# Performance work log

Hardware: AMD Instinct MI355X
Metric: run time of the kernel (lower is better)

The kernel has to match this reference:

```python
import jax, jax.numpy as jnp
import numpy as np

NUM_NODES = 100000
NUM_EDGES = 1600000
DIM = 64
NUM_LAYERS = 3


def setup_inputs() -> dict:
    key = jax.random.key(0)
    k1, k2 = jax.random.split(key)
    x = jax.random.normal(k1, (NUM_NODES, DIM), dtype=jnp.float32)
    adj_t = jax.random.randint(k2, (2, NUM_EDGES), 0, NUM_NODES, dtype=jnp.int64)
    return {"x": x, "adj_t": adj_t}


def reference(x, adj_t):
    n = x.shape[0]
    # undirected -> add reversed edges (adj_t_is_undirected=True path)
    edge_index = jnp.concatenate([adj_t, adj_t[::-1]], axis=1)  # [2, 2E]
    row, col = edge_index[0], edge_index[1]
    edge_weight = jnp.ones((row.shape[0],), dtype=x.dtype)
    # gcn_norm: D^-0.5 A D^-0.5 (degree computed by scatter over col)
    deg = jax.ops.segment_sum(edge_weight, col, num_segments=n)
    deg_inv_sqrt = jnp.where(deg > 0, jax.lax.rsqrt(deg), 0.0).astype(x.dtype)
    w = deg_inv_sqrt[row] * edge_weight * deg_inv_sqrt[col]  # [2E]
    outs = [x]
    for _ in range(NUM_LAYERS):
        # gather -> scale -> scatter_add (SpMM)
        msgs = w[:, None] * x[row]                     # [2E, D]
        x = jax.ops.segment_sum(msgs, col, num_segments=n)  # [N, D]
        outs.append(x)
    return jnp.mean(jnp.stack(outs), axis=0)
```

## Files before the change

kernel.cpp:

```cpp
#include <hip/hip_runtime.h>

#define DIM 64
#define BKT_SHIFT 7
#define BKT_G 128
#define NBLK 256
#define HIST_B 1024
#define SCAP (HIST_B * 8)
#define CAP 4608
#define RCAP 18

__device__ inline float blo(unsigned p) { return __uint_as_float(p << 16); }
__device__ inline float bhi(unsigned p) { return __uint_as_float(p & 0xffff0000u); }
__device__ inline unsigned bpack(float x, float y) {
    unsigned ux = __float_as_uint(x);
    unsigned uy = __float_as_uint(y);
    ux += 0x7fffu + ((ux >> 16) & 1u);
    uy += 0x7fffu + ((uy >> 16) & 1u);
    return (ux >> 16) | (uy & 0xffff0000u);
}

__global__ void zero_kernel(int* __restrict__ p, int n) {
    int i = blockIdx.x * blockDim.x + threadIdx.x;
    if (i < n) p[i] = 0;
}

__global__ __launch_bounds__(HIST_B)
void place_direct_kernel(const int* __restrict__ adj, int E,
                         int* __restrict__ gcnt,
                         unsigned* __restrict__ pairs, int NB) {
    extern __shared__ int L[];
    int* cnt    = L;
    int* lb     = L + NB;
    int* cur    = L + 2 * NB + 1;
    int* gb     = L + 3 * NB + 1;
    int* wsum   = L + 4 * NB + 1;
    int* staged = L + 4 * NB + 17;
    const int tid  = threadIdx.x;
    const int lane = tid & 63;
    const int wid  = tid >> 6;
    const int n4 = E >> 2;
    const int4* srcs = (const int4*)adj;
    const int4* dsts = (const int4*)(adj + E);
    const int nrounds = (n4 + NBLK * HIST_B - 1) / (NBLK * HIST_B);

    for (int r = 0; r < nrounds; ++r) {
        for (int g = tid; g < NB; g += HIST_B) cnt[g] = 0;
        __syncthreads();
        int i = (r * NBLK + blockIdx.x) * HIST_B + tid;
        int4 a = {0, 0, 0, 0}, b = {0, 0, 0, 0};
        int valid = 0;
        if (i < n4) {
            a = srcs[i];
            b = dsts[i];
            valid = 1;
            atomicAdd(&cnt[a.x >> BKT_SHIFT], 1);
            atomicAdd(&cnt[a.y >> BKT_SHIFT], 1);
            atomicAdd(&cnt[a.z >> BKT_SHIFT], 1);
            atomicAdd(&cnt[a.w >> BKT_SHIFT], 1);
            atomicAdd(&cnt[b.x >> BKT_SHIFT], 1);
            atomicAdd(&cnt[b.y >> BKT_SHIFT], 1);
            atomicAdd(&cnt[b.z >> BKT_SHIFT], 1);
            atomicAdd(&cnt[b.w >> BKT_SHIFT], 1);
        }
        __syncthreads();
        int v = (tid < NB) ? cnt[tid] : 0;
        int s = v;
#pragma unroll
        for (int off = 1; off < 64; off <<= 1) {
            int o = __shfl_up(s, off);
            if (lane >= off) s += o;
        }
        if (lane == 63) wsum[wid] = s;
        __syncthreads();
        if (wid == 0 && lane < 16) {
            int w = wsum[lane];
#pragma unroll
            for (int off = 1; off < 16; off <<= 1) {
                int o = __shfl_up(w, off);
                if (lane >= off) w += o;
            }
            wsum[lane] = w;
        }
        __syncthreads();
        int incl = s + (wid ? wsum[wid - 1] : 0);
        if (tid < NB) {
            lb[tid + 1] = incl;
            cur[tid] = incl - v;
            gb[tid]  = (v > 0) ? atomicAdd(&gcnt[tid], v) : 0;
        }
        if (tid == 0) lb[0] = 0;
        __syncthreads();
        int total = lb[NB];
        if (valid) {
#define STAGE_EMIT(av, bv)                                                     \
    {                                                                          \
        int g_ = (bv) >> BKT_SHIFT;                                            \
        int p_ = atomicAdd(&cur[g_], 1);                                       \
        staged[p_] = (int)(((unsigned)((bv) & (BKT_G - 1)) << 17) |            \
                           (unsigned)(av));                                    \
        g_ = (av) >> BKT_SHIFT;                                                \
        p_ = atomicAdd(&cur[g_], 1);                                           \
        staged[p_] = (int)(((unsigned)((av) & (BKT_G - 1)) << 17) |            \
                           (unsigned)(bv));                                    \
    }
            STAGE_EMIT(a.x, b.x); STAGE_EMIT(a.y, b.y);
            STAGE_EMIT(a.z, b.z); STAGE_EMIT(a.w, b.w);
#undef STAGE_EMIT
        }
        __syncthreads();
        for (int k = tid; k < total; k += HIST_B) {
            int lo = 0, hi = NB - 1;
            while (lo < hi) {
                int mid = (lo + hi + 1) >> 1;
                if (lb[mid] <= k) lo = mid; else hi = mid - 1;
            }
            int p = gb[lo] + (k - lb[lo]);
            if (p < CAP)
                pairs[(size_t)lo * CAP + p] = (unsigned)staged[k];
        }
        __syncthreads();
    }
    if (blockIdx.x == 0) {
        for (int e = (n4 << 2) + tid; e < E; e += HIST_B) {
            int av = adj[e], bv = adj[E + e];
            int g1 = bv >> BKT_SHIFT;
            int p1 = atomicAdd(&gcnt[g1], 1);
            if (p1 < CAP)
                pairs[(size_t)g1 * CAP + p1] =
                    ((unsigned)(bv & (BKT_G - 1)) << 17) | (unsigned)av;
            int g2 = av >> BKT_SHIFT;
            int p2 = atomicAdd(&gcnt[g2], 1);
            if (p2 < CAP)
                pairs[(size_t)g2 * CAP + p2] =
                    ((unsigned)(av & (BKT_G - 1)) << 17) | (unsigned)bv;
        }
    }
}

__global__ __launch_bounds__(256)
void pass2_build_kernel(const unsigned* __restrict__ pairs,
                        const int* __restrict__ gcnt,
                        const float4* __restrict__ x,
                        int* __restrict__ csr_src,
                        int* __restrict__ row_ptr,
                        int* __restrict__ deg,
                        float* __restrict__ dinv,
                        uint4* __restrict__ xs0,
                        int N, int NB, int total_adj) {
    __shared__ int cnt[BKT_G];
    __shared__ int pre[BKT_G];
    __shared__ int cur[BKT_G];
    __shared__ float dv[BKT_G];
    __shared__ int win[CAP];
    __shared__ int red[256];
    int g = blockIdx.x;
    int base = g << BKT_SHIFT;
    size_t poff = (size_t)g * CAP;
    int m = gcnt[g];
    if (m > CAP) m = CAP;
    int lsum = 0;
    for (int h = threadIdx.x; h < g; h += 256) lsum += gcnt[h];
    red[threadIdx.x] = lsum;
    if (threadIdx.x < BKT_G) cnt[threadIdx.x] = 0;
    __syncthreads();
    for (int o = 128; o > 0; o >>= 1) {
        if (threadIdx.x < o) red[threadIdx.x] += red[threadIdx.x + o];
        __syncthreads();
    }
    int coff = red[0];
    unsigned rec[RCAP];
#pragma unroll
    for (int k = 0; k < RCAP; ++k) {
        int i = threadIdx.x + k * 256;
        unsigned p = 0;
        if (i < m) {
            p = pairs[poff + i];
            atomicAdd(&cnt[p >> 17], 1);
        }
        rec[k] = p;
    }
    __syncthreads();
    if (threadIdx.x < BKT_G) pre[threadIdx.x] = cnt[threadIdx.x];
    __syncthreads();
    for (int o = 1; o < BKT_G; o <<= 1) {
        int t = 0;
        if (threadIdx.x < BKT_G && threadIdx.x >= o) t = pre[threadIdx.x - o];
        __syncthreads();
        if (threadIdx.x < BKT_G) pre[threadIdx.x] += t;
        __syncthreads();
    }
    if (threadIdx.x < BKT_G) {
        int v = base + threadIdx.x;
        if (v < N) {
            int c = cnt[threadIdx.x];
            int lstart = pre[threadIdx.x] - c;
            float di = (c > 0) ? rsqrtf((float)c) : 0.0f;
            row_ptr[v] = coff + lstart;
            deg[v] = c;
            dinv[v] = di;
            dv[threadIdx.x] = di;
            cur[threadIdx.x] = lstart;
        }
    }
    if (g == NB - 1 && threadIdx.x == 0) row_ptr[N] = total_adj;
    __syncthreads();
#pragma unroll
    for (int k = 0; k < RCAP; ++k) {
        int i = threadIdx.x + k * 256;
        if (i < m) {
            unsigned p = rec[k];
            int pos = atomicAdd(&cur[p >> 17], 1);
            win[pos] = (int)(p & 0x1ffffu);
        }
    }
    __syncthreads();
    for (int i = threadIdx.x; i < m; i += 256)
        csr_src[coff + i] = win[i];
    for (int w = threadIdx.x; w < BKT_G * 8; w += blockDim.x) {
        int vl = w >> 3, sub = w & 7;
        int v = base + vl;
        if (v < N) {
            float di = dv[vl];
            float4 xa = x[(size_t)v * 16 + sub * 2];
            float4 xb = x[(size_t)v * 16 + sub * 2 + 1];
            uint4 o;
            o.x = bpack(di * xa.x, di * xa.y);
            o.y = bpack(di * xa.z, di * xa.w);
            o.z = bpack(di * xb.x, di * xb.y);
            o.w = bpack(di * xb.z, di * xb.w);
            xs0[(size_t)v * 8 + sub] = o;
        }
    }
}

#define SPMM_ACCUM_BODY                                                        \
    int half = threadIdx.x & 31;                                               \
    int nb = half >> 3, sub = half & 7;                                        \
    int beg = row_ptr[v];                                                      \
    int end = row_ptr[v + 1];                                                  \
    int full = (end - beg) >> 4;                                               \
    float a0 = 0, a1 = 0, a2 = 0, a3 = 0, a4 = 0, a5 = 0, a6 = 0, a7 = 0;      \
    int j = beg;                                                               \
    int s0 = 0, s1 = 0, s2 = 0, s3 = 0;                                        \
    if (full > 0) {                                                            \
        int b = j + 4 * nb;                                                    \
        s0 = csr_src[b];     s1 = csr_src[b + 1];                              \
        s2 = csr_src[b + 2]; s3 = csr_src[b + 3];                              \
    }                                                                          \
    for (int it = 0; it < full; ++it) {                                        \
        int jn = j + 16;                                                       \
        int t0 = 0, t1 = 0, t2 = 0, t3 = 0;                                    \
        if (it + 1 < full) {                                                   \
            int b = jn + 4 * nb;                                               \
            t0 = csr_src[b];     t1 = csr_src[b + 1];                          \
            t2 = csr_src[b + 2]; t3 = csr_src[b + 3];                          \
        }                                                                      \
        uint4 p0 = xs_in[(size_t)s0 * 8 + sub];                                \
        uint4 p1 = xs_in[(size_t)s1 * 8 + sub];                                \
        uint4 p2 = xs_in[(size_t)s2 * 8 + sub];                                \
        uint4 p3 = xs_in[(size_t)s3 * 8 + sub];                                \
        a0 += (blo(p0.x) + blo(p1.x)) + (blo(p2.x) + blo(p3.x));               \
        a1 += (bhi(p0.x) + bhi(p1.x)) + (bhi(p2.x) + bhi(p3.x));               \
        a2 += (blo(p0.y) + blo(p1.y)) + (blo(p2.y) + blo(p3.y));               \
        a3 += (bhi(p0.y) + bhi(p1.y)) + (bhi(p2.y) + bhi(p3.y));               \
        a4 += (blo(p0.z) + blo(p1.z)) + (blo(p2.z) + blo(p3.z));               \
        a5 += (bhi(p0.z) + bhi(p1.z)) + (bhi(p2.z) + bhi(p3.z));               \
        a6 += (blo(p0.w) + blo(p1.w)) + (blo(p2.w) + blo(p3.w));               \
        a7 += (bhi(p0.w) + bhi(p1.w)) + (bhi(p2.w) + bhi(p3.w));               \
        s0 = t0; s1 = t1; s2 = t2; s3 = t3;                                    \
        j = jn;                                                                \
    }                                                                          \
    for (int idx = j + nb; idx < end; idx += 4) {                              \
        int s = csr_src[idx];                                                  \
        uint4 p = xs_in[(size_t)s * 8 + sub];                                  \
        a0 += blo(p.x); a1 += bhi(p.x);                                        \
        a2 += blo(p.y); a3 += bhi(p.y);                                        \
        a4 += blo(p.z); a5 += bhi(p.z);                                        \
        a6 += blo(p.w); a7 += bhi(p.w);                                        \
    }                                                                          \
    a0 += __shfl_xor(a0, 8);  a0 += __shfl_xor(a0, 16);                        \
    a1 += __shfl_xor(a1, 8);  a1 += __shfl_xor(a1, 16);                        \
    a2 += __shfl_xor(a2, 8);  a2 += __shfl_xor(a2, 16);                        \
    a3 += __shfl_xor(a3, 8);  a3 += __shfl_xor(a3, 16);                        \
    a4 += __shfl_xor(a4, 8);  a4 += __shfl_xor(a4, 16);                        \
    a5 += __shfl_xor(a5, 8);  a5 += __shfl_xor(a5, 16);                        \
    a6 += __shfl_xor(a6, 8);  a6 += __shfl_xor(a6, 16);                        \
    a7 += __shfl_xor(a7, 8);  a7 += __shfl_xor(a7, 16);

__global__ void spmm_bf16_kernel(const int* __restrict__ row_ptr,
                                 const int* __restrict__ csr_src,
                                 const float* __restrict__ dinv,
                                 const uint4* __restrict__ xs_in,
                                 uint4* __restrict__ xs_out, int N) {
    int t = blockIdx.x * blockDim.x + threadIdx.x;
    int v = t >> 5;
    if (v >= N) return;
    SPMM_ACCUM_BODY
    if (nb == 0) {
        float di = dinv[v];
        float d2 = di * di;
        uint4 o;
        o.x = bpack(d2 * a0, d2 * a1);
        o.y = bpack(d2 * a2, d2 * a3);
        o.z = bpack(d2 * a4, d2 * a5);
        o.w = bpack(d2 * a6, d2 * a7);
        xs_out[(size_t)v * 8 + sub] = o;
    }
}

__global__ void spmm_last_kernel(const int* __restrict__ row_ptr,
                                 const int* __restrict__ csr_src,
                                 const float* __restrict__ dinv,
                                 const int* __restrict__ deg,
                                 const uint4* __restrict__ xs_in,
                                 const uint4* __restrict__ xs1,
                                 const float4* __restrict__ x,
                                 float4* __restrict__ out, int N) {
    int t = blockIdx.x * blockDim.x + threadIdx.x;
    int v = t >> 5;
    if (v >= N) return;
    SPMM_ACCUM_BODY
    if (nb == 0) {
        float di = dinv[v];
        float rs = sqrtf((float)deg[v]);
        size_t idx = (size_t)v * 8 + sub;
        uint4 q1 = xs1[idx];
        uint4 q2 = xs_in[idx];
        float4 xa = x[(size_t)v * 16 + sub * 2];
        float4 xb = x[(size_t)v * 16 + sub * 2 + 1];
        float4 oa, ob;
        oa.x = 0.25f * (xa.x + rs * (blo(q1.x) + blo(q2.x)) + di * a0);
        oa.y = 0.25f * (xa.y + rs * (bhi(q1.x) + bhi(q2.x)) + di * a1);
        oa.z = 0.25f * (xa.z + rs * (blo(q1.y) + blo(q2.y)) + di * a2);
        oa.w = 0.25f * (xa.w + rs * (bhi(q1.y) + bhi(q2.y)) + di * a3);
        ob.x = 0.25f * (xb.x + rs * (blo(q1.z) + blo(q2.z)) + di * a4);
        ob.y = 0.25f * (xb.y + rs * (bhi(q1.z) + bhi(q2.z)) + di * a5);
        ob.z = 0.25f * (xb.z + rs * (blo(q1.w) + blo(q2.w)) + di * a6);
        ob.w = 0.25f * (xb.w + rs * (bhi(q1.w) + bhi(q2.w)) + di * a7);
        out[(size_t)v * 16 + sub * 2]     = oa;
        out[(size_t)v * 16 + sub * 2 + 1] = ob;
    }
}

extern "C" void kernel_launch(void* const* d_in, const int* in_sizes, int n_in,
                              void* d_out, int out_size, void* d_ws, size_t ws_size,
                              hipStream_t stream) {
    const float* x = (const float*)d_in[0];
    const int* adj = (const int*)d_in[1];
    float* out     = (float*)d_out;

    const int total_adj = in_sizes[1];
    const int E = total_adj / 2;
    const int N = in_sizes[0] / DIM;
    const int NB = (N + BKT_G - 1) / BKT_G;

    size_t BUF = (size_t)total_adj * 4;
    size_t xsb = (size_t)N * 32 * 4;
    if (xsb > BUF) BUF = xsb;
    BUF = (BUF + 255) & ~(size_t)255;
    size_t PAIRS_B = ((size_t)NB * CAP * 4 + 255) & ~(size_t)255;

    char* ws = (char*)d_ws;
    int*      deg     = (int*)(ws);
    float*    dinv    = (float*)(ws + (size_t)512 * 1024);
    int*      row_ptr = (int*)(ws + (size_t)1024 * 1024);
    int*      gcnt    = (int*)(ws + (size_t)1536 * 1024);
    char*     big     = ws + (size_t)1664 * 1024;
    int*      csr_src = (int*)(big);
    unsigned* pairs   = (unsigned*)(big + BUF);
    uint4*    xs0     = (uint4*)(big + BUF + PAIRS_B);
    uint4*    xs1     = (uint4*)(big + BUF + PAIRS_B + BUF);
    uint4*    xs2     = (uint4*)(big + BUF + PAIRS_B + 2 * BUF);

    const int B = 256;

    zero_kernel<<<(NB + 1023) / 1024, 1024, 0, stream>>>(gcnt, NB);

    size_t place_lds = (size_t)(4 * NB + 17 + SCAP) * sizeof(int);
    place_direct_kernel<<<NBLK, HIST_B, place_lds, stream>>>(adj, E, gcnt,
                                                             pairs, NB);

    pass2_build_kernel<<<NB, B, 0, stream>>>(pairs, gcnt, (const float4*)x,
                                             csr_src, row_ptr, deg, dinv,
                                             xs0, N, NB, total_adj);

    const int nblocks32 = (int)(((long long)N * 32 + B - 1) / B);
    spmm_bf16_kernel<<<nblocks32, B, 0, stream>>>(row_ptr, csr_src, dinv, xs0, xs1, N);
    spmm_bf16_kernel<<<nblocks32, B, 0, stream>>>(row_ptr, csr_src, dinv, xs1, xs2, N);
    spmm_last_kernel<<<nblocks32, B, 0, stream>>>(row_ptr, csr_src, dinv, deg,
                                                  xs2, xs1, (const float4*)x,
                                                  (float4*)out, N);
}
```

Before: 280.2 us.

## Sort CSR neighbors by source octant and gather per-octant for cache locality

The CSR build now sorts each row's neighbors by a 3-bit source-range key, splitting sources into 8 octants. It stores per-node octant prefix counts packed as bytes in a new qpre array. The SpMM kernels are rewritten so each block handles 64 nodes and walks the octants in order, with a block barrier between octants, so gathers of source features stay within one smaller slice of the feature table and should hit L2 more often. The thread mapping also changes to one 32-bit word (two bf16 features) per lane per node, in place of 16-byte vector loads split over neighbor quarters. The price is narrower loads, serial per-node edge loops, extra barriers, and byte-packed counts that overflow if a node's degree exceeds 255.

```diff
diff --git a/kernel.cpp b/kernel.cpp
--- a/kernel.cpp
+++ b/kernel.cpp
@@ -8,6 +8,8 @@
 #define SCAP (HIST_B * 8)
 #define CAP 4608
 #define RCAP 18
+#define NKEY (BKT_G * 8)
+#define NPB 64
 
 __device__ inline float blo(unsigned p) { return __uint_as_float(p << 16); }
 __device__ inline float bhi(unsigned p) { return __uint_as_float(p & 0xffff0000u); }
@@ -145,14 +147,16 @@
                         int* __restrict__ row_ptr,
                         int* __restrict__ deg,
                         float* __restrict__ dinv,
+                        uint2* __restrict__ qpre,
                         uint4* __restrict__ xs0,
                         int N, int NB, int total_adj) {
-    __shared__ int cnt[BKT_G];
-    __shared__ int pre[BKT_G];
-    __shared__ int cur[BKT_G];
+    __shared__ int cnt[NKEY];
+    __shared__ int pre[NKEY];
+    __shared__ int cur[NKEY];
     __shared__ float dv[BKT_G];
     __shared__ int win[CAP];
     __shared__ int red[256];
+    __shared__ int wsum4[4];
     int g = blockIdx.x;
     int base = g << BKT_SHIFT;
     size_t poff = (size_t)g * CAP;
@@ -161,7 +165,7 @@
     int lsum = 0;
     for (int h = threadIdx.x; h < g; h += 256) lsum += gcnt[h];
     red[threadIdx.x] = lsum;
-    if (threadIdx.x < BKT_G) cnt[threadIdx.x] = 0;
+    for (int kk = threadIdx.x; kk < NKEY; kk += 256) cnt[kk] = 0;
     __syncthreads();
     for (int o = 128; o > 0; o >>= 1) {
         if (threadIdx.x < o) red[threadIdx.x] += red[threadIdx.x + o];
@@ -175,31 +179,66 @@
         unsigned p = 0;
         if (i < m) {
             p = pairs[poff + i];
-            atomicAdd(&cnt[p >> 17], 1);
+            int key = (int)(((p >> 17) << 3) | ((p & 0x1ffffu) >> 14));
+            atomicAdd(&cnt[key], 1);
         }
         rec[k] = p;
     }
     __syncthreads();
-    if (threadIdx.x < BKT_G) pre[threadIdx.x] = cnt[threadIdx.x];
-    __syncthreads();
-    for (int o = 1; o < BKT_G; o <<= 1) {
-        int t = 0;
-        if (threadIdx.x < BKT_G && threadIdx.x >= o) t = pre[threadIdx.x - o];
-        __syncthreads();
-        if (threadIdx.x < BKT_G) pre[threadIdx.x] += t;
-        __syncthreads();
-    }
+    {
+        int lane = threadIdx.x & 63, wid = threadIdx.x >> 6;
+        int t4 = threadIdx.x << 2;
+        int c0 = cnt[t4], c1 = cnt[t4 + 1], c2 = cnt[t4 + 2], c3 = cnt[t4 + 3];
+        int i1 = c0 + c1, i2 = i1 + c2, i3 = i2 + c3;
+        int s = i3;
+#pragma unroll
+        for (int off = 1; off < 64; off <<= 1) {
+            int o = __shfl_up(s, off);
+            if (lane >= off) s += o;
+        }
+        if (lane == 63) wsum4[wid] = s;
+        __syncthreads();
+        if (threadIdx.x == 0) {
+            int w0 = wsum4[0], w1 = wsum4[1], w2 = wsum4[2];
+            wsum4[0] = 0; wsum4[1] = w0; wsum4[2] = w0 + w1;
+            wsum4[3] = w0 + w1 + w2;
+        }
+        __syncthreads();
+        int texc = wsum4[wid] + s - i3;
+        pre[t4]     = texc + c0;
+        pre[t4 + 1] = texc + i1;
+        pre[t4 + 2] = texc + i2;
+        pre[t4 + 3] = texc + i3;
+        cur[t4]     = texc;
+        cur[t4 + 1] = texc + c0;
+        cur[t4 + 2] = texc + i1;
+        cur[t4 + 3] = texc + i2;
+    }
+    __syncthreads();
     if (threadIdx.x < BKT_G) {
         int v = base + threadIdx.x;
         if (v < N) {
-            int c = cnt[threadIdx.x];
-            int lstart = pre[threadIdx.x] - c;
+            int k8 = threadIdx.x << 3;
+            int nstart = threadIdx.x ? pre[k8 - 1] : 0;
+            int b0 = pre[k8]     - nstart;
+            int b1 = pre[k8 + 1] - nstart;
+            int b2 = pre[k8 + 2] - nstart;
+            int b3 = pre[k8 + 3] - nstart;
+            int b4 = pre[k8 + 4] - nstart;
+            int b5 = pre[k8 + 5] - nstart;
+            int b6 = pre[k8 + 6] - nstart;
+            int b7 = pre[k8 + 7] - nstart;
+            int c = b7;
             float di = (c > 0) ? rsqrtf((float)c) : 0.0f;
-            row_ptr[v] = coff + lstart;
+            row_ptr[v] = coff + nstart;
             deg[v] = c;
             dinv[v] = di;
             dv[threadIdx.x] = di;
-            cur[threadIdx.x] = lstart;
+            qpre[v] = make_uint2(
+                (unsigned)b0 | ((unsigned)b1 << 8) | ((unsigned)b2 << 16) |
+                    ((unsigned)b3 << 24),
+                (unsigned)b4 | ((unsigned)b5 << 8) | ((unsigned)b6 << 16) |
+                    ((unsigned)b7 << 24));
         }
     }
     if (g == NB - 1 && threadIdx.x == 0) row_ptr[N] = total_adj;
@@ -209,7 +248,8 @@
         int i = threadIdx.x + k * 256;
         if (i < m) {
             unsigned p = rec[k];
-            int pos = atomicAdd(&cur[p >> 17], 1);
+            int key = (int)(((p >> 17) << 3) | ((p & 0x1ffffu) >> 14));
+            int pos = atomicAdd(&cur[key], 1);
             win[pos] = (int)(p & 0x1ffffu);
         }
     }
@@ -233,112 +273,110 @@
     }
 }
 
-#define SPMM_ACCUM_BODY                                                        \
-    int half = threadIdx.x & 31;                                               \
-    int nb = half >> 3, sub = half & 7;                                        \
-    int beg = row_ptr[v];                                                      \
-    int end = row_ptr[v + 1];                                                  \
-    int full = (end - beg) >> 4;                                               \
-    float a0 = 0, a1 = 0, a2 = 0, a3 = 0, a4 = 0, a5 = 0, a6 = 0, a7 = 0;      \
-    int j = beg;                                                               \
-    int s0 = 0, s1 = 0, s2 = 0, s3 = 0;                                        \
-    if (full > 0) {                                                            \
-        int b = j + 4 * nb;                                                    \
-        s0 = csr_src[b];     s1 = csr_src[b + 1];                              \
-        s2 = csr_src[b + 2]; s3 = csr_src[b + 3];                              \
+#define SPMM_OCT_GATHER                                                        \
+    int lane = threadIdx.x & 31;                                               \
+    int grp  = threadIdx.x >> 5;                                               \
+    float ax[8] = {0, 0, 0, 0, 0, 0, 0, 0};                                    \
+    float ay[8] = {0, 0, 0, 0, 0, 0, 0, 0};                                    \
+    for (int oct = 0; oct < 8; ++oct) {                                        \
+        _Pragma("unroll")                                                      \
+        for (int k = 0; k < 8; ++k) {                                          \
+            int ni = k * 8 + grp;                                              \
+            int v = v0 + ni;                                                   \
+            if (v < N) {                                                       \
+                unsigned long long Q =                                         \
+                    ((unsigned long long)qb[ni] << 32) | qa[ni];               \
+                int hi = (int)((Q >> (oct * 8)) & 255ull);                     \
+                int lo = oct ? (int)((Q >> (oct * 8 - 8)) & 255ull) : 0;       \
+                int bs = rp[ni] + lo;                                          \
+                int len = hi - lo;                                             \
+                int j = 0;                                                     \
+                for (; j + 4 <= len; j += 4) {                                 \
+                    int s0 = csr_src[bs + j];                                  \
+                    int s1 = csr_src[bs + j + 1];                              \
+                    int s2 = csr_src[bs + j + 2];                              \
+                    int s3 = csr_src[bs + j + 3];                              \
+                    unsigned u0 = xsw[(size_t)s0 * 32 + lane];                 \
+                    unsigned u1 = xsw[(size_t)s1 * 32 + lane];                 \
+                    unsigned u2 = xsw[(size_t)s2 * 32 + lane];                 \
+                    unsigned u3 = xsw[(size_t)s3 * 32 + lane];                 \
+                    ax[k] += (blo(u0) + blo(u1)) + (blo(u2) + blo(u3));        \
+                    ay[k] += (bhi(u0) + bhi(u1)) + (bhi(u2) + bhi(u3));        \
+                }                                                              \
+                for (; j < len; ++j) {                                         \
+                    int s = csr_src[bs + j];                                   \
+                    unsigned u = xsw[(size_t)s * 32 + lane];                   \
+                    ax[k] += blo(u);                                           \
+                    ay[k] += bhi(u);                                           \
+                }                                                              \
+            }                                                                  \
+        }                                                                      \
+        __syncthreads();                                                       \
+    }
+
+#define SPMM_OCT_PRELUDE                                                       \
+    __shared__ int rp[NPB];                                                    \
+    __shared__ unsigned qa[NPB], qb[NPB];                                      \
+    int v0 = blockIdx.x * NPB;                                                 \
+    for (int i = threadIdx.x; i < NPB; i += 256) {                             \
+        int v = v0 + i;                                                        \
+        rp[i] = (v < N) ? row_ptr[v] : 0;                                      \
+        uint2 q = (v < N) ? qpre[v] : make_uint2(0u, 0u);                      \
+        qa[i] = q.x;                                                           \
+        qb[i] = q.y;                                                           \
     }                                                                          \
-    for (int it = 0; it < full; ++it) {                                        \
-        int jn = j + 16;                                                       \
-        int t0 = 0, t1 = 0, t2 = 0, t3 = 0;                                    \
-        if (it + 1 < full) {                                                   \
-            int b = jn + 4 * nb;                                               \
-            t0 = csr_src[b];     t1 = csr_src[b + 1];                          \
-            t2 = csr_src[b + 2]; t3 = csr_src[b + 3];                          \
-        }                                                                      \
-        uint4 p0 = xs_in[(size_t)s0 * 8 + sub];                                \
-        uint4 p1 = xs_in[(size_t)s1 * 8 + sub];                                \
-        uint4 p2 = xs_in[(size_t)s2 * 8 + sub];                                \
-        uint4 p3 = xs_in[(size_t)s3 * 8 + sub];                                \
-        a0 += (blo(p0.x) + blo(p1.x)) + (blo(p2.x) + blo(p3.x));               \
-        a1 += (bhi(p0.x) + bhi(p1.x)) + (bhi(p2.x) + bhi(p3.x));               \
-        a2 += (blo(p0.y) + blo(p1.y)) + (blo(p2.y) + blo(p3.y));               \
-        a3 += (bhi(p0.y) + bhi(p1.y)) + (bhi(p2.y) + bhi(p3.y));               \
-        a4 += (blo(p0.z) + blo(p1.z)) + (blo(p2.z) + blo(p3.z));               \
-        a5 += (bhi(p0.z) + bhi(p1.z)) + (bhi(p2.z) + bhi(p3.z));               \
-        a6 += (blo(p0.w) + blo(p1.w)) + (blo(p2.w) + blo(p3.w));               \
-        a7 += (bhi(p0.w) + bhi(p1.w)) + (bhi(p2.w) + bhi(p3.w));               \
-        s0 = t0; s1 = t1; s2 = t2; s3 = t3;                                    \
-        j = jn;                                                                \
-    }                                                                          \
-    for (int idx = j + nb; idx < end; idx += 4) {                              \
-        int s = csr_src[idx];                                                  \
-        uint4 p = xs_in[(size_t)s * 8 + sub];                                  \
-        a0 += blo(p.x); a1 += bhi(p.x);                                        \
-        a2 += blo(p.y); a3 += bhi(p.y);                                        \
-        a4 += blo(p.z); a5 += bhi(p.z);                                        \
-        a6 += blo(p.w); a7 += bhi(p.w);                                        \
-    }                                                                          \
-    a0 += __shfl_xor(a0, 8);  a0 += __shfl_xor(a0, 16);                        \
-    a1 += __shfl_xor(a1, 8);  a1 += __shfl_xor(a1, 16);                        \
-    a2 += __shfl_xor(a2, 8);  a2 += __shfl_xor(a2, 16);                        \
-    a3 += __shfl_xor(a3, 8);  a3 += __shfl_xor(a3, 16);                        \
-    a4 += __shfl_xor(a4, 8);  a4 += __shfl_xor(a4, 16);                        \
-    a5 += __shfl_xor(a5, 8);  a5 += __shfl_xor(a5, 16);                        \
-    a6 += __shfl_xor(a6, 8);  a6 += __shfl_xor(a6, 16);                        \
-    a7 += __shfl_xor(a7, 8);  a7 += __shfl_xor(a7, 16);
-
-__global__ void spmm_bf16_kernel(const int* __restrict__ row_ptr,
-                                 const int* __restrict__ csr_src,
-                                 const float* __restrict__ dinv,
-                                 const uint4* __restrict__ xs_in,
-                                 uint4* __restrict__ xs_out, int N) {
-    int t = blockIdx.x * blockDim.x + threadIdx.x;
-    int v = t >> 5;
-    if (v >= N) return;
-    SPMM_ACCUM_BODY
-    if (nb == 0) {
-        float di = dinv[v];
-        float d2 = di * di;
-        uint4 o;
-        o.x = bpack(d2 * a0, d2 * a1);
-        o.y = bpack(d2 * a2, d2 * a3);
-        o.z = bpack(d2 * a4, d2 * a5);
-        o.w = bpack(d2 * a6, d2 * a7);
-        xs_out[(size_t)v * 8 + sub] = o;
-    }
-}
-
-__global__ void spmm_last_kernel(const int* __restrict__ row_ptr,
-                                 const int* __restrict__ csr_src,
-                                 const float* __restrict__ dinv,
-                                 const int* __restrict__ deg,
-                                 const uint4* __restrict__ xs_in,
-                                 const uint4* __restrict__ xs1,
-                                 const float4* __restrict__ x,
-                                 float4* __restrict__ out, int N) {
-    int t = blockIdx.x * blockDim.x + threadIdx.x;
-    int v = t >> 5;
-    if (v >= N) return;
-    SPMM_ACCUM_BODY
-    if (nb == 0) {
-        float di = dinv[v];
-        float rs = sqrtf((float)deg[v]);
-        size_t idx = (size_t)v * 8 + sub;
-        uint4 q1 = xs1[idx];
-        uint4 q2 = xs_in[idx];
-        float4 xa = x[(size_t)v * 16 + sub * 2];
-        float4 xb = x[(size_t)v * 16 + sub * 2 + 1];
-        float4 oa, ob;
-        oa.x = 0.25f * (xa.x + rs * (blo(q1.x) + blo(q2.x)) + di * a0);
-        oa.y = 0.25f * (xa.y + rs * (bhi(q1.x) + bhi(q2.x)) + di * a1);
-        oa.z = 0.25f * (xa.z + rs * (blo(q1.y) + blo(q2.y)) + di * a2);
-        oa.w = 0.25f * (xa.w + rs * (bhi(q1.y) + bhi(q2.y)) + di * a3);
-        ob.x = 0.25f * (xb.x + rs * (blo(q1.z) + blo(q2.z)) + di * a4);
-        ob.y = 0.25f * (xb.y + rs * (bhi(q1.z) + bhi(q2.z)) + di * a5);
-        ob.z = 0.25f * (xb.z + rs * (blo(q1.w) + blo(q2.w)) + di * a6);
-        ob.w = 0.25f * (xb.w + rs * (bhi(q1.w) + bhi(q2.w)) + di * a7);
-        out[(size_t)v * 16 + sub * 2]     = oa;
-        out[(size_t)v * 16 + sub * 2 + 1] = ob;
+    __syncthreads();
+
+__global__ __launch_bounds__(256, 6)
+void spmm_oct_kernel(const int* __restrict__ row_ptr,
+                     const uint2* __restrict__ qpre,
+                     const int* __restrict__ csr_src,
+                     const float* __restrict__ dinv,
+                     const unsigned* __restrict__ xsw,
+                     unsigned* __restrict__ xow,
+                     int N) {
+    SPMM_OCT_PRELUDE
+    SPMM_OCT_GATHER
+#pragma unroll
+    for (int k = 0; k < 8; ++k) {
+        int ni = k * 8 + grp;
+        int v = v0 + ni;
+        if (v < N) {
+            float di = dinv[v];
+            float d2 = di * di;
+            xow[(size_t)v * 32 + lane] = bpack(d2 * ax[k], d2 * ay[k]);
+        }
+    }
+}
+
+__global__ __launch_bounds__(256, 6)
+void spmm_oct_last_kernel(const int* __restrict__ row_ptr,
+                          const uint2* __restrict__ qpre,
+                          const int* __restrict__ csr_src,
+                          const float* __restrict__ dinv,
+                          const int* __restrict__ deg,
+                          const unsigned* __restrict__ xsw,
+                          const unsigned* __restrict__ xs1w,
+                          const float2* __restrict__ x2,
+                          float2* __restrict__ out2, int N) {
+    SPMM_OCT_PRELUDE
+    SPMM_OCT_GATHER
+#pragma unroll
+    for (int k = 0; k < 8; ++k) {
+        int ni = k * 8 + grp;
+        int v = v0 + ni;
+        if (v < N) {
+            float di = dinv[v];
+            float rs = sqrtf((float)deg[v]);
+            size_t ri = (size_t)v * 32 + lane;
+            unsigned q1 = xs1w[ri];
+            unsigned q2 = xsw[ri];
+            float2 xv = x2[ri];
+            float2 o;
+            o.x = 0.25f * (xv.x + rs * (blo(q1) + blo(q2)) + di * ax[k]);
+            o.y = 0.25f * (xv.y + rs * (bhi(q1) + bhi(q2)) + di * ay[k]);
+            out2[ri] = o;
+        }
     }
 }
 
@@ -365,7 +403,8 @@
     float*    dinv    = (float*)(ws + (size_t)512 * 1024);
     int*      row_ptr = (int*)(ws + (size_t)1024 * 1024);
     int*      gcnt    = (int*)(ws + (size_t)1536 * 1024);
-    char*     big     = ws + (size_t)1664 * 1024;
+    uint2*    qpre    = (uint2*)(ws + (size_t)1600 * 1024);
+    char*     big     = ws + (size_t)2432 * 1024;
     int*      csr_src = (int*)(big);
     unsigned* pairs   = (unsigned*)(big + BUF);
     uint4*    xs0     = (uint4*)(big + BUF + PAIRS_B);
@@ -382,12 +421,18 @@
 
     pass2_build_kernel<<<NB, B, 0, stream>>>(pairs, gcnt, (const float4*)x,
                                              csr_src, row_ptr, deg, dinv,
-                                             xs0, N, NB, total_adj);
-
-    const int nblocks32 = (int)(((long long)N * 32 + B - 1) / B);
-    spmm_bf16_kernel<<<nblocks32, B, 0, stream>>>(row_ptr, csr_src, dinv, xs0, xs1, N);
-    spmm_bf16_kernel<<<nblocks32, B, 0, stream>>>(row_ptr, csr_src, dinv, xs1, xs2, N);
-    spmm_last_kernel<<<nblocks32, B, 0, stream>>>(row_ptr, csr_src, dinv, deg,
-                                                  xs2, xs1, (const float4*)x,
-                                                  (float4*)out, N);
-}
+                                             qpre, xs0, N, NB, total_adj);
+
+    const int nsp = (N + NPB - 1) / NPB;
+    spmm_oct_kernel<<<nsp, B, 0, stream>>>(row_ptr, qpre, csr_src, dinv,
+                                           (const unsigned*)xs0,
+                                           (unsigned*)xs1, N);
+    spmm_oct_kernel<<<nsp, B, 0, stream>>>(row_ptr, qpre, csr_src, dinv,
+                                           (const unsigned*)xs1,
+                                           (unsigned*)xs2, N);
+    spmm_oct_last_kernel<<<nsp, B, 0, stream>>>(row_ptr, qpre, csr_src, dinv,
+                                                deg, (const unsigned*)xs2,
+                                                (const unsigned*)xs1,
+                                                (const float2*)x,
+                                                (float2*)out, N);
+}
```

Result: slower. 491.6 us (+75.4%).
